# Kernel optimization log

Measured on AMD Instinct MI355X. Metric: run time of the kernel, lower is better.

## Reference

```python
import jax, jax.numpy as jnp
import numpy as np

BATCH = 4096
DIM_X = 256


def setup_inputs() -> dict:
    key = jax.random.key(0)
    k1, k2 = jax.random.split(key)
    inputs = jax.random.normal(k1, (BATCH, DIM_X), dtype=jnp.float32)
    # learned density-matrix parameter (original inits to zeros; use small randn
    # so the quadratic form is non-degenerate for testing)
    rho = jax.random.normal(k2, (DIM_X, DIM_X), dtype=jnp.float32) * 0.02
    return {"inputs": inputs, "rho": rho}


def reference(inputs, rho):
    # oper[b,i,k] = x_i * conj(x_k)  -> [B, d, d] outer product per sample
    oper = jnp.einsum('...i,...j->...ij', inputs, jnp.conj(inputs))
    # trace-style double contraction with rho: sum_{i,k,m} oper[b,i,k] rho[k,m] oper[b,m,i]
    # algebraically equals ||x||^2 * (x^H rho x), but computed as in the source.
    rho_res = jnp.einsum('...ik,km,...mi->...', oper, rho, oper)
    return rho_res
```

## Files before the change

kernel.cpp:

```cpp
#include <hip/hip_runtime.h>

#define BATCH 4096
#define DIM   256
#define ROWS  64
#define NSPLIT 4
#define PAD_DIM 264

typedef __attribute__((ext_vector_type(8))) short short8;
typedef __attribute__((ext_vector_type(4))) float f32x4;

__device__ inline short f32_to_bf16(float f) {
    union { float f; unsigned u; } v; v.f = f;
    unsigned r = (v.u + 0x7FFFu + ((v.u >> 16) & 1u)) >> 16;
    return (short)r;
}
__device__ inline float bf16_to_f32(unsigned short s) {
    union { unsigned u; float f; } v; v.u = ((unsigned)s) << 16;
    return v.f;
}

__global__ __launch_bounds__(512, 2) void qmd_kernel(
    const float* __restrict__ X,
    const float* __restrict__ rho,
    float* __restrict__ out)
{
    __shared__ unsigned short xbf[ROWS][PAD_DIM];
    __shared__ float red_q[ROWS][8];
    __shared__ float red_s[ROWS];

    const int tid  = threadIdx.x;
    const int wave = tid >> 6;
    const int lane = tid & 63;
    const int quad = lane >> 4;
    const int lrow = lane & 15;
    const int r0   = (blockIdx.x >> 2) * ROWS;
    const int n0   = (blockIdx.x & 3) * 64;

    {
        const int srow = tid >> 3;
        const int scol = tid & 7;
        const float4* xrow4 = (const float4*)(X + (size_t)(r0 + srow) * DIM);
        float s2 = 0.f;
        #pragma unroll
        for (int j = 0; j < 8; ++j) {
            float4 v = xrow4[scol + 8 * j];
            s2 += v.x * v.x + v.y * v.y + v.z * v.z + v.w * v.w;
            short4 b;
            b.x = f32_to_bf16(v.x); b.y = f32_to_bf16(v.y);
            b.z = f32_to_bf16(v.z); b.w = f32_to_bf16(v.w);
            *(short4*)&xbf[srow][(scol + 8 * j) * 4] = b;
        }
        s2 += __shfl_xor(s2, 1, 64);
        s2 += __shfl_xor(s2, 2, 64);
        s2 += __shfl_xor(s2, 4, 64);
        if ((tid & 7) == 0) red_s[srow] = s2;
    }
    __syncthreads();

    const int k0 = wave * 32 + quad * 8;

    f32x4 acc[4][4];
    #pragma unroll
    for (int m = 0; m < 4; ++m)
        #pragma unroll
        for (int n = 0; n < 4; ++n)
            acc[m][n] = (f32x4){0.f, 0.f, 0.f, 0.f};

    short8 afr[4];
    #pragma unroll
    for (int mt = 0; mt < 4; ++mt)
        afr[mt] = *(const short8*)&xbf[mt * 16 + lrow][k0];

    short8 bfr[4];
    #pragma unroll
    for (int nt = 0; nt < 4; ++nt) {
        const int n = n0 + nt * 16 + lrow;
        const float* bp = rho + (size_t)n * DIM + k0;
        float4 b0 = *(const float4*)bp;
        float4 b1 = *(const float4*)(bp + 4);
        short8 b;
        b[0] = f32_to_bf16(b0.x); b[1] = f32_to_bf16(b0.y);
        b[2] = f32_to_bf16(b0.z); b[3] = f32_to_bf16(b0.w);
        b[4] = f32_to_bf16(b1.x); b[5] = f32_to_bf16(b1.y);
        b[6] = f32_to_bf16(b1.z); b[7] = f32_to_bf16(b1.w);
        bfr[nt] = b;
    }

    #pragma unroll
    for (int mt = 0; mt < 4; ++mt)
        #pragma unroll
        for (int nt = 0; nt < 4; ++nt)
            acc[mt][nt] = __builtin_amdgcn_mfma_f32_16x16x32_bf16(
                afr[mt], bfr[nt], acc[mt][nt], 0, 0, 0);

    #pragma unroll
    for (int mt = 0; mt < 4; ++mt)
        #pragma unroll
        for (int rg = 0; rg < 4; ++rg) {
            const int row = mt * 16 + quad * 4 + rg;
            float q = 0.f;
            #pragma unroll
            for (int nt = 0; nt < 4; ++nt)
                q += acc[mt][nt][rg] *
                     bf16_to_f32(xbf[row][n0 + nt * 16 + lrow]);
            q += __shfl_xor(q, 1, 64);
            q += __shfl_xor(q, 2, 64);
            q += __shfl_xor(q, 4, 64);
            q += __shfl_xor(q, 8, 64);
            if (lrow == 0) red_q[row][wave] = q;
        }
    __syncthreads();

    if (tid < ROWS) {
        float q = 0.f;
        #pragma unroll
        for (int w = 0; w < 8; ++w) q += red_q[tid][w];
        atomicAdd(&out[r0 + tid], q * red_s[tid]);
    }
}

extern "C" void kernel_launch(void* const* d_in, const int* in_sizes, int n_in,
                              void* d_out, int out_size, void* d_ws, size_t ws_size,
                              hipStream_t stream) {
    const float* X   = (const float*)d_in[0];
    const float* rho = (const float*)d_in[1];
    float* out = (float*)d_out;
    qmd_kernel<<<(BATCH / ROWS) * NSPLIT, 512, 0, stream>>>(X, rho, out);
}
```

Measured before the change: 62.94 us.

## Halve row tile, stage rho in LDS, transpose MFMA output for cheaper reduction

Row tile drops from 64 to 32 and blocks from 512 to 256 threads, doubling the grid. Each wave now covers 64 of the K dimension with two MFMA k-steps. A 64-row rho slice is converted to bf16 with the packed v_cvt_pk_bf16_f32 instruction and staged cooperatively in LDS, replacing per-lane strided global loads. The MFMA is issued as rho×x so each lane holds contiguous n values for one row, which turns the 4-step cross-lane reduction into 2 shuffles. In exchange, each block reloads a rho slice, and twice as many blocks fetch it, so rho traffic grows.

```diff
diff --git a/kernel.cpp b/kernel.cpp
--- a/kernel.cpp
+++ b/kernel.cpp
@@ -2,30 +2,32 @@
 
 #define BATCH 4096
 #define DIM   256
-#define ROWS  64
+#define ROWS  32
 #define NSPLIT 4
-#define PAD_DIM 264
+#define PAD   264
 
 typedef __attribute__((ext_vector_type(8))) short short8;
 typedef __attribute__((ext_vector_type(4))) float f32x4;
+typedef __attribute__((ext_vector_type(4))) unsigned short ushort4v;
 
-__device__ inline short f32_to_bf16(float f) {
-    union { float f; unsigned u; } v; v.f = f;
-    unsigned r = (v.u + 0x7FFFu + ((v.u >> 16) & 1u)) >> 16;
-    return (short)r;
+__device__ inline unsigned cvt_pk_bf16(float lo, float hi) {
+    unsigned r;
+    asm("v_cvt_pk_bf16_f32 %0, %1, %2" : "=v"(r) : "v"(lo), "v"(hi));
+    return r;
 }
 __device__ inline float bf16_to_f32(unsigned short s) {
     union { unsigned u; float f; } v; v.u = ((unsigned)s) << 16;
     return v.f;
 }
 
-__global__ __launch_bounds__(512, 2) void qmd_kernel(
+__global__ __launch_bounds__(256, 2) void qmd_kernel(
     const float* __restrict__ X,
     const float* __restrict__ rho,
     float* __restrict__ out)
 {
-    __shared__ unsigned short xbf[ROWS][PAD_DIM];
-    __shared__ float red_q[ROWS][8];
+    __shared__ unsigned short xbf[ROWS][PAD];
+    __shared__ unsigned short rbf[64][PAD];
+    __shared__ float red_q[ROWS][4];
     __shared__ float red_s[ROWS];
 
     const int tid  = threadIdx.x;
@@ -45,76 +47,85 @@
         for (int j = 0; j < 8; ++j) {
             float4 v = xrow4[scol + 8 * j];
             s2 += v.x * v.x + v.y * v.y + v.z * v.z + v.w * v.w;
-            short4 b;
-            b.x = f32_to_bf16(v.x); b.y = f32_to_bf16(v.y);
-            b.z = f32_to_bf16(v.z); b.w = f32_to_bf16(v.w);
-            *(short4*)&xbf[srow][(scol + 8 * j) * 4] = b;
+            unsigned p0 = cvt_pk_bf16(v.x, v.y);
+            unsigned p1 = cvt_pk_bf16(v.z, v.w);
+            *(uint2*)&xbf[srow][(scol + 8 * j) * 4] = make_uint2(p0, p1);
         }
         s2 += __shfl_xor(s2, 1, 64);
         s2 += __shfl_xor(s2, 2, 64);
         s2 += __shfl_xor(s2, 4, 64);
         if ((tid & 7) == 0) red_s[srow] = s2;
     }
+
+    {
+        const int srow = tid >> 3;
+        const int scol = tid & 7;
+        #pragma unroll
+        for (int h = 0; h < 2; ++h) {
+            const int rr = h * 32 + srow;
+            const float4* rrow4 = (const float4*)(rho + (size_t)(n0 + rr) * DIM);
+            #pragma unroll
+            for (int j = 0; j < 8; ++j) {
+                float4 v = rrow4[scol + 8 * j];
+                unsigned p0 = cvt_pk_bf16(v.x, v.y);
+                unsigned p1 = cvt_pk_bf16(v.z, v.w);
+                *(uint2*)&rbf[rr][(scol + 8 * j) * 4] = make_uint2(p0, p1);
+            }
+        }
+    }
     __syncthreads();
 
-    const int k0 = wave * 32 + quad * 8;
+    f32x4 accT[4][2];
+    #pragma unroll
+    for (int nt = 0; nt < 4; ++nt)
+        #pragma unroll
+        for (int mt = 0; mt < 2; ++mt)
+            accT[nt][mt] = (f32x4){0.f, 0.f, 0.f, 0.f};
 
-    f32x4 acc[4][4];
+    short8 afr[2][2];
     #pragma unroll
-    for (int m = 0; m < 4; ++m)
+    for (int mt = 0; mt < 2; ++mt)
         #pragma unroll
-        for (int n = 0; n < 4; ++n)
-            acc[m][n] = (f32x4){0.f, 0.f, 0.f, 0.f};
+        for (int ks = 0; ks < 2; ++ks)
+            afr[mt][ks] = *(const short8*)
+                &xbf[mt * 16 + lrow][wave * 64 + ks * 32 + quad * 8];
 
-    short8 afr[4];
+    short8 bfr[4][2];
     #pragma unroll
-    for (int mt = 0; mt < 4; ++mt)
-        afr[mt] = *(const short8*)&xbf[mt * 16 + lrow][k0];
-
-    short8 bfr[4];
-    #pragma unroll
-    for (int nt = 0; nt < 4; ++nt) {
-        const int n = n0 + nt * 16 + lrow;
-        const float* bp = rho + (size_t)n * DIM + k0;
-        float4 b0 = *(const float4*)bp;
-        float4 b1 = *(const float4*)(bp + 4);
-        short8 b;
-        b[0] = f32_to_bf16(b0.x); b[1] = f32_to_bf16(b0.y);
-        b[2] = f32_to_bf16(b0.z); b[3] = f32_to_bf16(b0.w);
-        b[4] = f32_to_bf16(b1.x); b[5] = f32_to_bf16(b1.y);
-        b[6] = f32_to_bf16(b1.z); b[7] = f32_to_bf16(b1.w);
-        bfr[nt] = b;
-    }
+    for (int nt = 0; nt < 4; ++nt)
+        #pragma unroll
+        for (int ks = 0; ks < 2; ++ks)
+            bfr[nt][ks] = *(const short8*)
+                &rbf[nt * 16 + lrow][wave * 64 + ks * 32 + quad * 8];
 
     #pragma unroll
-    for (int mt = 0; mt < 4; ++mt)
+    for (int nt = 0; nt < 4; ++nt)
         #pragma unroll
-        for (int nt = 0; nt < 4; ++nt)
-            acc[mt][nt] = __builtin_amdgcn_mfma_f32_16x16x32_bf16(
-                afr[mt], bfr[nt], acc[mt][nt], 0, 0, 0);
+        for (int mt = 0; mt < 2; ++mt)
+            #pragma unroll
+            for (int ks = 0; ks < 2; ++ks)
+                accT[nt][mt] = __builtin_amdgcn_mfma_f32_16x16x32_bf16(
+                    bfr[nt][ks], afr[mt][ks], accT[nt][mt], 0, 0, 0);
 
     #pragma unroll
-    for (int mt = 0; mt < 4; ++mt)
+    for (int mt = 0; mt < 2; ++mt) {
+        float q = 0.f;
         #pragma unroll
-        for (int rg = 0; rg < 4; ++rg) {
-            const int row = mt * 16 + quad * 4 + rg;
-            float q = 0.f;
+        for (int nt = 0; nt < 4; ++nt) {
+            ushort4v xv = *(const ushort4v*)
+                &xbf[mt * 16 + lrow][n0 + nt * 16 + quad * 4];
             #pragma unroll
-            for (int nt = 0; nt < 4; ++nt)
-                q += acc[mt][nt][rg] *
-                     bf16_to_f32(xbf[row][n0 + nt * 16 + lrow]);
-            q += __shfl_xor(q, 1, 64);
-            q += __shfl_xor(q, 2, 64);
-            q += __shfl_xor(q, 4, 64);
-            q += __shfl_xor(q, 8, 64);
-            if (lrow == 0) red_q[row][wave] = q;
+            for (int rg = 0; rg < 4; ++rg)
+                q += accT[nt][mt][rg] * bf16_to_f32(xv[rg]);
         }
+        q += __shfl_xor(q, 16, 64);
+        q += __shfl_xor(q, 32, 64);
+        if (lane < 16) red_q[mt * 16 + lane][wave] = q;
+    }
     __syncthreads();
 
     if (tid < ROWS) {
-        float q = 0.f;
-        #pragma unroll
-        for (int w = 0; w < 8; ++w) q += red_q[tid][w];
+        float q = red_q[tid][0] + red_q[tid][1] + red_q[tid][2] + red_q[tid][3];
         atomicAdd(&out[r0 + tid], q * red_s[tid]);
     }
 }
@@ -125,5 +136,5 @@
     const float* X   = (const float*)d_in[0];
     const float* rho = (const float*)d_in[1];
     float* out = (float*)d_out;
-    qmd_kernel<<<(BATCH / ROWS) * NSPLIT, 512, 0, stream>>>(X, rho, out);
+    qmd_kernel<<<(BATCH / ROWS) * NSPLIT, 256, 0, stream>>>(X, rho, out);
 }
```

After: 58.49 us. 7.1% less time.
